# Kernel optimization log

Hardware: AMD Instinct MI355X
Metric: run time of the kernel (lower is better)

The kernel has to match this reference:

```python
import jax, jax.numpy as jnp
import numpy as np
import math

H, M, N = 64, 128, 128  # volume dims (m == n required by original index math)
K_NEIGH = 9
W_WIN = 3


def build_neighbor_ids(h, n, w):
    # Periodic (wrap-around) neighbor indices, matching extract_neighbour_indices
    # with m == n. Loop order: z-major, then y, then x, offsets -1..1 for w=3.
    half = w // 2
    offs = list(range(-half, half + 1))
    zi = jnp.arange(h)[:, None, None]
    yi = jnp.arange(n)[None, :, None]
    xi = jnp.arange(n)[None, None, :]
    cols = []
    for oz in offs:
        for oy in offs:
            for ox in offs:
                idx = ((zi + oz) % h) * (n * n) + ((yi + oy) % n) * n + ((xi + ox) % n)
                cols.append(idx.reshape(-1))
    return jnp.stack(cols, axis=1).astype(jnp.int32)  # [P, w^3]


def setup_inputs() -> dict:
    key = jax.random.key(0)
    k1, _ = jax.random.split(key)
    inp = jax.random.normal(k1, (H, M, N), dtype=jnp.float32)
    ksigma = jnp.ones((1, 1, 1, 1), dtype=jnp.float32)  # nn.Parameter init to sigma_m=1.0
    return {"input": inp, "ksigma": ksigma, "k": K_NEIGH, "w": W_WIN}


def reference(input, ksigma, k, w):
    h, m, n = input.shape
    ID = build_neighbor_ids(h, n, w)               # [P, nN]
    anat = input.reshape(-1)                       # [P]
    # get_knn: absolute intensity differences to each neighbor
    dist = jnp.abs(anat[ID] - anat[:, None])       # [P, nN]
    order = jnp.argsort(dist, axis=-1, stable=True)
    sID = jnp.take_along_axis(ID, order, axis=1)   # sorted neighbor indices
    IDk = sID[:, :k]                               # [P, k] top-k nearest by intensity
    Wk = anat[IDk]                                 # [P, k] neighbor intensities (feature rows)
    # get_features: per-row std (torch.std is unbiased, ddof=1)
    sigma = jnp.std(Wk, axis=1, ddof=1)            # [P]
    sigma_safe = jnp.where(sigma == 0, 1.0, sigma)
    neigh = Wk[IDk]                                # [P, k, k] gather feature rows of knn
    diff = Wk[:, None, :] - neigh + 1e-6           # pairwise_distance eps added to diff
    norm = jnp.sqrt(jnp.sum(diff * diff, axis=-1)) # [P, k] L2 pairwise distance
    ks = ksigma.reshape(())
    logits = -jnp.square(norm / sigma_safe[:, None] / (math.sqrt(2.0) * ks))
    logits = jnp.where(sigma[:, None] == 0, 0.0, logits)  # zero row -> uniform softmax
    Kw = jax.nn.softmax(logits, axis=1)            # [P, k] normalized kernel weights
    return Kw
```

## Files before the change

### kernel.cpp

```cpp
#include <hip/hip_runtime.h>
#include <hip/hip_fp16.h>
#include <array>

constexpr int HZ   = 64;
constexpr int NN   = 128;
constexpr int P    = HZ * NN * NN;
constexpr int KSEL = 9;
constexpr int NCOL = 27;

typedef _Float16 f16x2 __attribute__((ext_vector_type(2)));

constexpr int CZ = 8, CY = 8, CX = 16;
constexpr int NCORE = CZ * CY * CX;
constexpr int RZ = 10, RY = 10, RX = 18;
constexpr int NROWS = RZ * RY * RX;
constexpr int NHALO = NROWS - NCORE;
constexpr int IZ = 12, IY = 12, IXW = 24;
constexpr int NIN = IZ * IY * IXW;
constexpr int NIN16 = IZ * IY * (IXW / 4);

constexpr int compute_nce(int n) {
  int t = 0; while ((1 << t) < n) ++t;
  int cnt = 0;
  for (int p = 1 << (t - 1); p > 0; p >>= 1) {
    int q = 1 << (t - 1), r = 0, d = p;
    while (true) {
      for (int i = 0; i < n - d; ++i)
        if ((i & p) == r) ++cnt;
      if (q == p) break;
      d = q - p; r = p; q >>= 1;
    }
  }
  return cnt;
}
constexpr int NCE_FULL = compute_nce(NCOL);

struct CEPair { unsigned char a, b; };
constexpr std::array<CEPair, NCE_FULL> make_net() {
  std::array<CEPair, NCE_FULL> net{};
  int t = 0; while ((1 << t) < NCOL) ++t;
  int k = 0;
  for (int p = 1 << (t - 1); p > 0; p >>= 1) {
    int q = 1 << (t - 1), r = 0, d = p;
    while (true) {
      for (int i = 0; i < NCOL - d; ++i)
        if ((i & p) == r) {
          net[k].a = (unsigned char)i;
          net[k].b = (unsigned char)(i + d);
          ++k;
        }
      if (q == p) break;
      d = q - p; r = p; q >>= 1;
    }
  }
  return net;
}
constexpr auto FULLNET = make_net();

constexpr int count_pruned() {
  bool needed[NCOL] = {};
  for (int i = 0; i < KSEL; ++i) needed[i] = true;
  int cnt = 0;
  for (int e = NCE_FULL - 1; e >= 0; --e) {
    const int a = FULLNET[e].a, b = FULLNET[e].b;
    if (needed[a] || needed[b]) { needed[a] = true; needed[b] = true; ++cnt; }
  }
  return cnt;
}
constexpr int NCE = count_pruned();

constexpr std::array<CEPair, NCE> make_pruned() {
  bool needed[NCOL] = {};
  for (int i = 0; i < KSEL; ++i) needed[i] = true;
  std::array<bool, NCE_FULL> keep{};
  for (int e = NCE_FULL - 1; e >= 0; --e) {
    const int a = FULLNET[e].a, b = FULLNET[e].b;
    if (needed[a] || needed[b]) { keep[e] = true; needed[a] = true; needed[b] = true; }
  }
  std::array<CEPair, NCE> out{};
  int k = 0;
  for (int e = 0; e < NCE_FULL; ++e) if (keep[e]) out[k++] = FULLNET[e];
  return out;
}
constexpr auto NET = make_pruned();

constexpr std::array<unsigned short, NHALO> make_halo() {
  std::array<unsigned short, NHALO> t{};
  int k = 0;
  for (int r = 0; r < NROWS; ++r) {
    const int rz = r / (RY * RX), rem = r % (RY * RX);
    const int ry = rem / RX, rx = rem % RX;
    const bool core = (rz >= 1 && rz <= CZ) && (ry >= 1 && ry <= CY) &&
                      (rx >= 1 && rx <= CX);
    if (!core) t[k++] = (unsigned short)r;
  }
  return t;
}
__device__ constexpr auto HALO = make_halo();

typedef const __attribute__((address_space(1))) unsigned GU;
typedef __attribute__((address_space(3))) unsigned LU;

__device__ __forceinline__ void g2l16(const void* g, void* l) {
  __builtin_amdgcn_global_load_lds((GU*)g, (LU*)l, 16, 0, 0);
}

template <bool COLS>
__device__ __forceinline__ void sort_row(
    const float* __restrict__ in_t, int rz, int ry, int rx,
    unsigned od[4], unsigned& h8, unsigned& lo, unsigned& hi) {
  const float center = in_t[((rz + 1) * IY + (ry + 1)) * IXW + rx + 3];

  unsigned long long key[NCOL];
  #pragma unroll
  for (int c = 0; c < NCOL; ++c) {
    const int czi = c / 9, cyi = (c / 3) % 3, cxi = c % 3;
    const float v = in_t[((rz + czi) * IY + (ry + cyi)) * IXW + rx + cxi + 2];
    const unsigned vb = __float_as_uint(v);
    const unsigned db = __float_as_uint(v - center) & 0x7fffffffu;
    key[c] = ((unsigned long long)db << 32) |
             (((unsigned)c << 27) | (vb >> 5));
  }

  #pragma unroll
  for (int e = 0; e < NCE; ++e) {
    const int a = NET[e].a, b = NET[e].b;
    const double ka = __builtin_bit_cast(double, key[a]);
    const double kb = __builtin_bit_cast(double, key[b]);
    key[a] = __builtin_bit_cast(unsigned long long, fmin(ka, kb));
    key[b] = __builtin_bit_cast(unsigned long long, fmax(ka, kb));
  }

  od[0] = od[1] = od[2] = od[3] = 0; h8 = 0; lo = 0; hi = 0;
  #pragma unroll
  for (int k = 0; k < KSEL; ++k) {
    const unsigned kl = (unsigned)key[k];
    const unsigned vbits = (kl & 0x07ffffffu) << 5;
    const unsigned hb = (unsigned)__half_as_ushort(__float2half(__uint_as_float(vbits)));
    if (k < 8) od[k >> 1] |= hb << ((k & 1) * 16);
    else       h8 = hb;
    if (COLS) {
      const unsigned c = (kl >> 27) & 31u;
      if (k < 6) lo |= c << (5 * k);
      else       hi |= c << (5 * (k - 6));
    }
  }
}

__global__ __launch_bounds__(512) void buildk_fused6(
    const float* __restrict__ anat,
    const float* __restrict__ ksig,
    float* __restrict__ out) {
  __shared__ __align__(16) unsigned char ldsb[NROWS * 16 + NROWS * 2 + NIN * 4];
  unsigned*       tA   = (unsigned*)ldsb;
  unsigned short* tB0h = (unsigned short*)(ldsb + NROWS * 16);
  float*          in_t = (float*)(ldsb + NROWS * 16 + NROWS * 2);

  const int tid = threadIdx.x;

  const int blk = blockIdx.x;
  const int swz = ((blk & 7) << 7) | (blk >> 3);
  const int zt   = swz >> 7;
  const int rest = swz & 127;
  const int y0   = ((rest >> 3) & 15) << 3;
  const int x0   = (rest & 7) << 4;
  const int z0   = zt << 3;

  const int xl = tid & 15;
  const int yl = (tid >> 4) & 7;
  const int zl = tid >> 7;

  #pragma unroll
  for (int s = 0; s < 2; ++s) {
    const unsigned q = (unsigned)(s * 512 + tid);
    if (q < (unsigned)NIN16) {
      const unsigned p = q / 6u;
      const unsigned t = q - 6u * p;
      const unsigned iz = p / 12u;
      const unsigned iy = p - 12u * iz;
      const int zz = (z0 + (int)iz - 2) & (HZ - 1);
      const int yy = (y0 + (int)iy - 2) & (NN - 1);
      const int xb = (x0 - 4 + 4 * (int)t) & (NN - 1);
      g2l16(&anat[(zz << 14) | (yy << 7) | xb], &in_t[q * 4]);
    }
  }
  __syncthreads();

  unsigned lo0, hi0, lo1, hi1;
  {
    unsigned od[4], h8;
    const int rz = 2 * zl + 1, ry = yl + 1, rx = xl + 1;
    const int ru = (rz * RY + ry) * RX + rx;
    sort_row<true>(in_t, rz, ry, rx, od, h8, lo0, hi0);
    *(uint4*)&tA[(unsigned)ru * 4] = make_uint4(od[0], od[1], od[2], od[3]);
    tB0h[ru] = (unsigned short)h8;
  }
  {
    unsigned od[4], h8;
    const int rz = 2 * zl + 2, ry = yl + 1, rx = xl + 1;
    const int ru = (rz * RY + ry) * RX + rx;
    sort_row<true>(in_t, rz, ry, rx, od, h8, lo1, hi1);
    *(uint4*)&tA[(unsigned)ru * 4] = make_uint4(od[0], od[1], od[2], od[3]);
    tB0h[ru] = (unsigned short)h8;
  }
  #pragma unroll 1
  for (int s = 0; s < 2; ++s) {
    const int idx = s * 512 + tid;
    if (idx < NHALO) {
      const int ru = (int)HALO[idx];
      const int rz = ru / (RY * RX);
      const int rem = ru - (RY * RX) * rz;
      const int ry = rem / RX, rx = rem - RX * ry;
      unsigned od[4], h8, lo, hi;
      sort_row<false>(in_t, rz, ry, rx, od, h8, lo, hi);
      *(uint4*)&tA[(unsigned)ru * 4] = make_uint4(od[0], od[1], od[2], od[3]);
      tB0h[ru] = (unsigned short)h8;
    }
  }
  __syncthreads();

  const float ks = ksig[0];
  const _Float16 epsh = (_Float16)1e-6f;
  const f16x2 eps2 = {epsh, epsh};

  float res[2][9];

  #pragma unroll
  for (int vz = 0; vz < 2; ++vz) {
    const int zv = 2 * zl + vz;
    const unsigned lo = (vz == 0) ? lo0 : lo1;
    const unsigned hi = (vz == 0) ? hi0 : hi1;

    const int rho_own = ((zv + 1) * RY + (yl + 1)) * RX + (xl + 1);
    const uint4 a = *(const uint4*)&tA[rho_own * 4];
    const unsigned b0 = (unsigned)tB0h[rho_own];
    f16x2 wh[5];
    wh[0] = __builtin_bit_cast(f16x2, a.x);
    wh[1] = __builtin_bit_cast(f16x2, a.y);
    wh[2] = __builtin_bit_cast(f16x2, a.z);
    wh[3] = __builtin_bit_cast(f16x2, a.w);
    wh[4] = __builtin_bit_cast(f16x2, b0);

    int rho[KSEL];
    #pragma unroll
    for (int j = 0; j < KSEL; ++j) {
      const unsigned c = (j < 6) ? ((lo >> (5 * j)) & 31u)
                                 : ((hi >> (5 * (j - 6))) & 31u);
      const unsigned czi = (c * 57u) >> 9;
      const unsigned rem = c - 9u * czi;
      const unsigned cyi = (rem * 11u) >> 5;
      const unsigned cxi = rem - 3u * cyi;
      rho[j] = ((zv + (int)czi) * RY + (yl + (int)cyi)) * RX + (xl + (int)cxi);
    }
    uint4 na[KSEL];
    unsigned nb[KSEL];
    #pragma unroll
    for (int j = 0; j < KSEL; ++j) {
      na[j] = *(const uint4*)&tA[rho[j] * 4];
      nb[j] = (unsigned)tB0h[rho[j]];
    }

    float ws[KSEL];
    #pragma unroll
    for (int l = 0; l < KSEL; ++l) ws[l] = (float)wh[l >> 1][l & 1];
    float mean = 0.f;
    #pragma unroll
    for (int l = 0; l < KSEL; ++l) mean += ws[l];
    mean *= (1.0f / 9.0f);
    float var = 0.f;
    #pragma unroll
    for (int l = 0; l < KSEL; ++l) { const float t = ws[l] - mean; var += t * t; }
    var *= (1.0f / 8.0f);
    const float sigma = sqrtf(var);

    const float inv2 = (sigma == 0.f)
        ? 0.f
        : 1.4426950408889634f / (2.0f * ks * ks * sigma * sigma);

    float logit[KSEL];
    #pragma unroll
    for (int j = 0; j < KSEL; ++j) {
      const f16x2 nh0 = __builtin_bit_cast(f16x2, na[j].x);
      const f16x2 nh1 = __builtin_bit_cast(f16x2, na[j].y);
      const f16x2 nh2 = __builtin_bit_cast(f16x2, na[j].z);
      const f16x2 nh3 = __builtin_bit_cast(f16x2, na[j].w);
      const f16x2 nh4 = __builtin_bit_cast(f16x2, nb[j]);
      float s = 0.f;
      f16x2 dd;
      dd = (wh[0] - nh0) + eps2; s = __builtin_amdgcn_fdot2(dd, dd, s, false);
      dd = (wh[1] - nh1) + eps2; s = __builtin_amdgcn_fdot2(dd, dd, s, false);
      dd = (wh[2] - nh2) + eps2; s = __builtin_amdgcn_fdot2(dd, dd, s, false);
      dd = (wh[3] - nh3) + eps2; s = __builtin_amdgcn_fdot2(dd, dd, s, false);
      dd = (wh[4] - nh4) + eps2; s = __builtin_amdgcn_fdot2(dd, dd, s, false);
      logit[j] = -s * inv2;
    }

    float mx = logit[0];
    #pragma unroll
    for (int j = 1; j < KSEL; ++j) mx = fmaxf(mx, logit[j]);
    float sum = 0.f;
    float e[KSEL];
    #pragma unroll
    for (int j = 0; j < KSEL; ++j) { e[j] = exp2f(logit[j] - mx); sum += e[j]; }
    const float rs = 1.0f / sum;
    #pragma unroll
    for (int j = 0; j < KSEL; ++j) res[vz][j] = e[j] * rs;
  }

  __syncthreads();
  float* tf = (float*)ldsb;
  #pragma unroll
  for (int vz = 0; vz < 2; ++vz) {
    const int zv = 2 * zl + vz;
    const int pos = (zv << 7) + (yl << 4) + xl;
    #pragma unroll
    for (int j = 0; j < KSEL; ++j) tf[pos * KSEL + j] = res[vz][j];
  }
  __syncthreads();

  const float4* tf4 = (const float4*)ldsb;
  #pragma unroll
  for (int s = 0; s < 5; ++s) {
    const unsigned q = (unsigned)(s * 512 + tid);
    if (q < 2304u) {
      const unsigned row = q / 36u;
      const unsigned f   = q - row * 36u;
      const int zz = z0 + (int)(row >> 3);
      const int yr = (int)(row & 7u);
      const unsigned vb = (unsigned)((zz << 14) | ((y0 + yr) << 7) | x0);
      ((float4*)out)[(size_t)(vb >> 2) * 9 + f] = tf4[row * 36 + f];
    }
  }
}

extern "C" void kernel_launch(void* const* d_in, const int* in_sizes, int n_in,
                              void* d_out, int out_size, void* d_ws, size_t ws_size,
                              hipStream_t stream) {
  const float* anat = (const float*)d_in[0];
  const float* ksig = (const float*)d_in[1];
  buildk_fused6<<<P / NCORE, 512, 0, stream>>>(anat, ksig, (float*)d_out);
}
```

Baseline: 103.1 us.

## Write softmax outputs directly to global and reorder neighbor loads by z-plane

Drops the LDS staging pass for the output, along with its two block barriers. Each thread now writes its 9 softmax weights straight to global memory instead of going through a coalesced float4 copy-out. The sort_row neighbor loads are regrouped by z-plane, with the center plane loaded first so the center value is available early, which may reduce register pressure or load latency. The direct per-thread stores are strided by 36 bytes, so global write coalescing is likely worse.

```diff
diff --git a/kernel.cpp b/kernel.cpp
--- a/kernel.cpp
+++ b/kernel.cpp
@@ -109,17 +109,41 @@
 __device__ __forceinline__ void sort_row(
     const float* __restrict__ in_t, int rz, int ry, int rx,
     unsigned od[4], unsigned& h8, unsigned& lo, unsigned& hi) {
-  const float center = in_t[((rz + 1) * IY + (ry + 1)) * IXW + rx + 3];
+  const int base = (rz * IY + ry) * IXW + rx + 2;
 
   unsigned long long key[NCOL];
-  #pragma unroll
-  for (int c = 0; c < NCOL; ++c) {
-    const int czi = c / 9, cyi = (c / 3) % 3, cxi = c % 3;
-    const float v = in_t[((rz + czi) * IY + (ry + cyi)) * IXW + rx + cxi + 2];
-    const unsigned vb = __float_as_uint(v);
-    const unsigned db = __float_as_uint(v - center) & 0x7fffffffu;
-    key[c] = ((unsigned long long)db << 32) |
-             (((unsigned)c << 27) | (vb >> 5));
+
+  float v1[9];
+  #pragma unroll
+  for (int cy = 0; cy < 3; ++cy)
+    #pragma unroll
+    for (int cx = 0; cx < 3; ++cx)
+      v1[cy * 3 + cx] = in_t[base + (IY + cy) * IXW + cx];
+  const float center = v1[4];
+
+  #pragma unroll
+  for (int i = 0; i < 9; ++i) {
+    const unsigned c = 9u + (unsigned)i;
+    const unsigned vb = __float_as_uint(v1[i]);
+    const unsigned db = __float_as_uint(v1[i] - center) & 0x7fffffffu;
+    key[c] = ((unsigned long long)db << 32) | ((c << 27) | (vb >> 5));
+  }
+  #pragma unroll
+  for (int pz = 0; pz < 2; ++pz) {
+    const int czi = pz * 2;
+    float vp[9];
+    #pragma unroll
+    for (int cy = 0; cy < 3; ++cy)
+      #pragma unroll
+      for (int cx = 0; cx < 3; ++cx)
+        vp[cy * 3 + cx] = in_t[base + (czi * IY + cy) * IXW + cx];
+    #pragma unroll
+    for (int i = 0; i < 9; ++i) {
+      const unsigned c = (unsigned)(czi * 9 + i);
+      const unsigned vb = __float_as_uint(vp[i]);
+      const unsigned db = __float_as_uint(vp[i] - center) & 0x7fffffffu;
+      key[c] = ((unsigned long long)db << 32) | ((c << 27) | (vb >> 5));
+    }
   }
 
   #pragma unroll
@@ -147,7 +171,7 @@
   }
 }
 
-__global__ __launch_bounds__(512) void buildk_fused6(
+__global__ __launch_bounds__(512) void buildk_fused7(
     const float* __restrict__ anat,
     const float* __restrict__ ksig,
     float* __restrict__ out) {
@@ -222,8 +246,6 @@
   const float ks = ksig[0];
   const _Float16 epsh = (_Float16)1e-6f;
   const f16x2 eps2 = {epsh, epsh};
-
-  float res[2][9];
 
   #pragma unroll
   for (int vz = 0; vz < 2; ++vz) {
@@ -303,33 +325,12 @@
     #pragma unroll
     for (int j = 0; j < KSEL; ++j) { e[j] = exp2f(logit[j] - mx); sum += e[j]; }
     const float rs = 1.0f / sum;
-    #pragma unroll
-    for (int j = 0; j < KSEL; ++j) res[vz][j] = e[j] * rs;
-  }
-
-  __syncthreads();
-  float* tf = (float*)ldsb;
-  #pragma unroll
-  for (int vz = 0; vz < 2; ++vz) {
-    const int zv = 2 * zl + vz;
-    const int pos = (zv << 7) + (yl << 4) + xl;
-    #pragma unroll
-    for (int j = 0; j < KSEL; ++j) tf[pos * KSEL + j] = res[vz][j];
-  }
-  __syncthreads();
-
-  const float4* tf4 = (const float4*)ldsb;
-  #pragma unroll
-  for (int s = 0; s < 5; ++s) {
-    const unsigned q = (unsigned)(s * 512 + tid);
-    if (q < 2304u) {
-      const unsigned row = q / 36u;
-      const unsigned f   = q - row * 36u;
-      const int zz = z0 + (int)(row >> 3);
-      const int yr = (int)(row & 7u);
-      const unsigned vb = (unsigned)((zz << 14) | ((y0 + yr) << 7) | x0);
-      ((float4*)out)[(size_t)(vb >> 2) * 9 + f] = tf4[row * 36 + f];
-    }
+
+    const unsigned vb = (unsigned)(((z0 + zv) << 14) | ((y0 + yl) << 7) |
+                                   (x0 + xl));
+    float* op = out + (size_t)vb * 9;
+    #pragma unroll
+    for (int j = 0; j < KSEL; ++j) op[j] = e[j] * rs;
   }
 }
 
@@ -338,5 +339,5 @@
                               hipStream_t stream) {
   const float* anat = (const float*)d_in[0];
   const float* ksig = (const float*)d_in[1];
-  buildk_fused6<<<P / NCORE, 512, 0, stream>>>(anat, ksig, (float*)d_out);
-}
+  buildk_fused7<<<P / NCORE, 512, 0, stream>>>(anat, ksig, (float*)d_out);
+}
```

Measured after the change: 101.6 us. About the same (-1.4%).
